# Kernel tuning notes

Measured on AMD Instinct MI355X. Metric: run time of the kernel, lower is better.

## Reference

```python
import jax, jax.numpy as jnp
import numpy as np

B, LQ, LK, D, H = 4, 1024, 1024, 512, 8


def setup_inputs() -> dict:
    key = jax.random.key(0)
    ks = jax.random.split(key, 6)
    # xavier_normal for (D, D): std = sqrt(2 / (D + D))
    std_qkv = (2.0 / (D + D)) ** 0.5
    std_p = (2.0 / (H * D + D)) ** 0.5
    x = jax.random.normal(ks[0], (B, LQ, D), dtype=jnp.float32)
    states = jax.random.normal(ks[1], (B, LK, D), dtype=jnp.float32)
    mask = jnp.ones((B, LQ, LK), dtype=jnp.int32)
    # per-head full-size QKV weights, stacked over heads: [H, D, D]
    Wq = jax.random.normal(ks[2], (H, D, D), dtype=jnp.float32) * std_qkv
    Wk = jax.random.normal(ks[3], (H, D, D), dtype=jnp.float32) * std_qkv
    Wv = jax.random.normal(ks[4], (H, D, D), dtype=jnp.float32) * std_qkv
    Wp = jax.random.normal(ks[5], (D, H * D), dtype=jnp.float32) * std_p
    return {"x": x, "states": states, "mask": mask,
            "Wq": Wq, "Wk": Wk, "Wv": Wv, "Wp": Wp}


def reference(x, states, mask, Wq, Wk, Wv, Wp):
    # Per-head linear projections (nn.Linear: y = x @ W.T), batched over heads.
    q = jnp.einsum('bld,hed->bhle', x, Wq)        # [B,H,Lq,D]
    k = jnp.einsum('bsd,hed->bhse', states, Wk)   # [B,H,Lk,D]
    v = jnp.einsum('bsd,hed->bhse', states, Wv)   # [B,H,Lk,D]
    scale = 1.0 / (D ** 0.5)
    scores = jnp.einsum('bhle,bhse->bhls', q, k) * scale  # [B,H,Lq,Lk]
    scores = jnp.where(mask[:, None, :, :] == 0, -jnp.inf, scores)
    attn = jax.nn.softmax(scores, axis=-1)
    # Original does broadcast multiply + sum; mathematically this is attn @ v.
    ctx = jnp.einsum('bhls,bhse->bhle', attn, v)  # [B,H,Lq,D]
    # torch.cat over heads in order -> head-major last dim
    ctx = jnp.transpose(ctx, (0, 2, 1, 3)).reshape(B, LQ, H * D)
    return ctx @ Wp.T  # [B,Lq,D]
```

## Files before the change

### kernel.cpp

```cpp
#include <hip/hip_runtime.h>
#include <hip/hip_bf16.h>
#include <cstdint>
#include <cstddef>


typedef __bf16 bf16;
typedef __bf16 bf16x4 __attribute__((ext_vector_type(4)));
typedef __bf16 bf16x8 __attribute__((ext_vector_type(8)));
typedef float f32x4 __attribute__((ext_vector_type(4)));

__device__ inline void gload_lds16(const void* g, void* l) {
  __builtin_amdgcn_global_load_lds(
      (const __attribute__((address_space(1))) void*)g,
      (__attribute__((address_space(3))) void*)l, 16, 0, 0);
}

template <typename CT, int MODE>
__device__ __forceinline__ void gemm_body(
    bf16* As, bf16* Bs,
    const bf16* __restrict__ A, const bf16* __restrict__ B, CT* __restrict__ C,
    int K, int lda, int ldb, int ldc, int m0, int n0, float scale,
    const unsigned* __restrict__ mrow, float* __restrict__ sumrow)
{
  const int t = threadIdx.x;
  const int lane = t & 63, w = t >> 6;
  const int wm = w >> 1, wn = w & 1;

  const int srow = t >> 3;
  const int schunk = (t & 7) ^ (srow & 7);
  const bf16* Ag = A + (size_t)(m0 + srow) * lda + schunk * 8;
  const bf16* Bg = B + (size_t)(n0 + srow) * ldb + schunk * 8;
  bf16* Als = As + t * 8;
  bf16* Bls = Bs + t * 8;

  f32x4 acc[4][4] = {};
  const int rr = lane & 15;
  const int q4 = lane >> 4;

  const int kIters = K >> 6;
  for (int kt = 0; kt < kIters; ++kt) {
    __syncthreads();
#pragma unroll
    for (int i = 0; i < 4; ++i) {
      gload_lds16(Ag + (size_t)(32 * i) * lda, Als + i * 2048);
      gload_lds16(Bg + (size_t)(32 * i) * ldb, Bls + i * 2048);
    }
    Ag += 64; Bg += 64;
    __syncthreads();

#pragma unroll
    for (int kk = 0; kk < 2; ++kk) {
      bf16x8 af[4], bfr[4];
      const int ck = kk * 4 + q4;
#pragma unroll
      for (int r = 0; r < 4; ++r) {
        const int R = wm * 64 + r * 16 + rr;
        af[r] = *(const bf16x8*)(As + R * 64 + ((ck ^ (R & 7)) << 3));
      }
#pragma unroll
      for (int c = 0; c < 4; ++c) {
        const int R = wn * 64 + c * 16 + rr;
        bfr[c] = *(const bf16x8*)(Bs + R * 64 + ((ck ^ (R & 7)) << 3));
      }
#pragma unroll
      for (int r = 0; r < 4; ++r)
#pragma unroll
        for (int c = 0; c < 4; ++c)
          acc[r][c] = __builtin_amdgcn_mfma_f32_16x16x32_bf16(af[r], bfr[c], acc[r][c], 0, 0, 0);
    }
  }

  if (MODE == 0) {
#pragma unroll
    for (int r = 0; r < 4; ++r) {
#pragma unroll
      for (int c = 0; c < 4; ++c) {
        const int gr0 = m0 + wm * 64 + r * 16 + (q4 << 2);
        const int gc = n0 + wn * 64 + c * 16 + rr;
#pragma unroll
        for (int i = 0; i < 4; ++i)
          C[(size_t)(gr0 + i) * ldc + gc] = (CT)(acc[r][c][i] * scale);
      }
    }
  } else {
    const int cb0 = (n0 + wn * 64) >> 5;
#pragma unroll
    for (int r = 0; r < 4; ++r) {
#pragma unroll
      for (int i = 0; i < 4; ++i) {
        const int row = m0 + wm * 64 + r * 16 + (q4 << 2) + i;
        const unsigned mw0 = mrow[(row << 5) + cb0];
        const unsigned mw1 = mrow[(row << 5) + cb0 + 1];
        float ps = 0.0f;
#pragma unroll
        for (int c = 0; c < 4; ++c) {
          const int gc = n0 + wn * 64 + c * 16 + rr;
          const unsigned mw = (c >= 2) ? mw1 : mw0;
          const unsigned bit = (mw >> (((c & 1) << 4) + rr)) & 1u;
          float p = bit ? __expf(acc[r][c][i] * scale) : 0.0f;
          C[(size_t)row * ldc + gc] = (CT)p;
          ps += p;
        }
        ps += __shfl_xor(ps, 1); ps += __shfl_xor(ps, 2);
        ps += __shfl_xor(ps, 4); ps += __shfl_xor(ps, 8);
        if (rr == 0) atomicAdd(sumrow + row, ps);
      }
    }
  }
}

__global__ __launch_bounds__(256) void prep_kernel(
    const float* __restrict__ x, const float* __restrict__ st,
    const float* __restrict__ Wp, const float* __restrict__ Wq,
    const float* __restrict__ Wk, const float* __restrict__ Wv,
    const int* __restrict__ mask,
    bf16* __restrict__ xb, bf16* __restrict__ stb, bf16* __restrict__ wpb,
    bf16* __restrict__ WqT, bf16* __restrict__ WkT, bf16* __restrict__ WvT,
    unsigned* __restrict__ mbits, float* __restrict__ sums)
{
  const int lin = blockIdx.x;
  const int t = threadIdx.x;
  if (lin < 6144) {
    const float* s; bf16* d;
    switch (lin >> 11) {
      case 0: s = x; d = xb; break;
      case 1: s = st; d = stb; break;
      default: s = Wp; d = wpb; break;
    }
    const int i = ((lin & 2047) * 256 + t) * 4;
    float4 v = *(const float4*)(s + i);
    bf16x4 o;
    o[0] = (bf16)v.x; o[1] = (bf16)v.y; o[2] = (bf16)v.z; o[3] = (bf16)v.w;
    *(bf16x4*)(d + i) = o;
  } else if (lin < 12288) {
    const int tid = lin - 6144;
    const float* s; bf16* d;
    switch (tid >> 11) {
      case 0: s = Wq; d = WqT; break;
      case 1: s = Wk; d = WkT; break;
      default: s = Wv; d = WvT; break;
    }
    const int gid = (tid & 2047) * 256 + t;
    const int e0 = (gid & 127) * 4;
    const int dd = (gid >> 7) & 511;
    const int h = gid >> 16;
    const float* src = s + (size_t)h * 262144 + (size_t)e0 * 512 + dd;
    bf16x4 o;
    o[0] = (bf16)src[0];
    o[1] = (bf16)src[512];
    o[2] = (bf16)src[1024];
    o[3] = (bf16)src[1536];
    *(bf16x4*)(d + (size_t)h * 262144 + (size_t)dd * 512 + e0) = o;
  } else if (lin < 12800) {
    const int gid = (lin - 12288) * 256 + t;
    const int* src = mask + (size_t)gid * 32;
    unsigned bits = 0;
#pragma unroll
    for (int j = 0; j < 32; j += 4) {
      int4 v = *(const int4*)(src + j);
      if (v.x) bits |= 1u << j;
      if (v.y) bits |= 1u << (j + 1);
      if (v.z) bits |= 1u << (j + 2);
      if (v.w) bits |= 1u << (j + 3);
    }
    mbits[gid] = bits;
  } else {
    const int i = ((lin - 12800) * 256 + t) * 4;
    *(float4*)(sums + i) = make_float4(0.f, 0.f, 0.f, 0.f);
  }
}

__global__ __launch_bounds__(256) void combine_kernel(
    const bf16* __restrict__ WqT, const bf16* __restrict__ WkT,
    const bf16* __restrict__ wpb, const bf16* __restrict__ WvT,
    bf16* __restrict__ Mt, bf16* __restrict__ U)
{
  __shared__ bf16 As[128 * 64];
  __shared__ bf16 Bs[128 * 64];
  const int bid = blockIdx.x;
  const int g = (bid & 7) * 32 + (bid >> 3);
  const int h = (g >> 4) & 7;
  const int tile = g & 15;
  if (g < 128) {
    gemm_body<bf16, 0>(As, Bs, WkT + (size_t)h * 262144, WqT + (size_t)h * 262144,
        Mt + (size_t)h * 262144, 512, 512, 512, 512,
        (tile >> 2) * 128, (tile & 3) * 128, 1.0f, nullptr, nullptr);
  } else {
    gemm_body<bf16, 0>(As, Bs, wpb + (size_t)h * 512, WvT + (size_t)h * 262144,
        U + (size_t)h * 262144, 512, 4096, 512, 512,
        (tile >> 2) * 128, (tile & 3) * 128, 1.0f, nullptr, nullptr);
  }
}

__global__ __launch_bounds__(256) void stage2_kernel(
    const bf16* __restrict__ xb, const bf16* __restrict__ stb,
    const bf16* __restrict__ Mt, const bf16* __restrict__ U,
    bf16* __restrict__ tq, bf16* __restrict__ VWT)
{
  __shared__ bf16 As[128 * 64];
  __shared__ bf16 Bs[128 * 64];
  const int bid = blockIdx.x;
  const int g = (bid & 7) * 256 + (bid >> 3);
  if (g < 1024) {
    const int z = g >> 5;
    const int tile = g & 31;
    const size_t zb = z >> 3, zh = z & 7;
    gemm_body<bf16, 0>(As, Bs, xb + zb * 524288, Mt + zh * 262144,
        tq + (size_t)z * 524288, 512, 512, 512, 512,
        (tile >> 2) * 128, (tile & 3) * 128, 1.0f, nullptr, nullptr);
  } else {
    const int g2 = g - 1024;
    const int z = g2 >> 5;
    const int j = g2 & 31;
    const size_t zb = z >> 3, zh = z & 7;
    gemm_body<bf16, 0>(As, Bs, U + zh * 262144, stb + zb * 524288,
        VWT + zb * 4194304 + zh * 524288, 512, 512, 512, 1024,
        (j >> 3) * 128, (j & 7) * 128, 1.0f, nullptr, nullptr);
  }
}

__global__ __launch_bounds__(256) void big_kernel(
    const bf16* __restrict__ tq, const bf16* __restrict__ stb,
    bf16* __restrict__ P,
    const unsigned* __restrict__ mbits, float* __restrict__ sums, float scale)
{
  __shared__ bf16 As[128 * 64];
  __shared__ bf16 Bs[128 * 64];
  const int bid = blockIdx.x;
  const int g = (bid & 7) * 256 + (bid >> 3);
  const int z = g >> 6;
  const int j = g & 63;
  const size_t zb = z >> 3, zh = z & 7;
  gemm_body<bf16, 1>(As, Bs,
      tq + (size_t)z * 524288,
      stb + zb * 524288,
      P + zb * 8388608 + zh * 1048576,
      512, 512, 512, 1024,
      (j >> 3) * 128, (j & 7) * 128, scale,
      mbits + (zb << 15), sums + ((size_t)z << 10));
}

__global__ __launch_bounds__(256) void pvw_kernel(
    const bf16* __restrict__ P, const bf16* __restrict__ VWT,
    const float* __restrict__ sums, float* __restrict__ part)
{
  __shared__ bf16 As[128 * 64];
  __shared__ bf16 Bs[128 * 64];
  const int lin = blockIdx.x;
  const int z = ((lin >> 8) << 3) | (lin & 7);
  const int j = (lin >> 3) & 31;
  const int zb = z >> 2, hp = z & 3;
  const int m0 = (j >> 2) * 128, n0 = (j & 3) * 128;
  const int t = threadIdx.x;
  const int lane = t & 63, w = t >> 6;
  const int wm = w >> 1, wn = w & 1;
  const int srow = t >> 3, schunk = (t & 7) ^ (srow & 7);
  const int rr = lane & 15, q4 = lane >> 4;
  bf16* Als = As + t * 8;
  bf16* Bls = Bs + t * 8;

  f32x4 accO[4][4] = {};

#pragma unroll
  for (int hh = 0; hh < 2; ++hh) {
    const int h = hp * 2 + hh;
    const bf16* Ag = P + (size_t)zb * 8388608 + (size_t)h * 1048576
                       + (size_t)(m0 + srow) * 1024 + schunk * 8;
    const bf16* Bg = VWT + (size_t)zb * 4194304 + (size_t)h * 524288
                        + (size_t)(n0 + srow) * 1024 + schunk * 8;
    f32x4 acc[4][4] = {};
    for (int kt = 0; kt < 16; ++kt) {
      __syncthreads();
#pragma unroll
      for (int i = 0; i < 4; ++i) {
        gload_lds16(Ag + (size_t)(32 * i) * 1024, Als + i * 2048);
        gload_lds16(Bg + (size_t)(32 * i) * 1024, Bls + i * 2048);
      }
      Ag += 64; Bg += 64;
      __syncthreads();
#pragma unroll
      for (int kk = 0; kk < 2; ++kk) {
        bf16x8 af[4], bfr[4];
        const int ck = kk * 4 + q4;
#pragma unroll
        for (int r = 0; r < 4; ++r) {
          const int R = wm * 64 + r * 16 + rr;
          af[r] = *(const bf16x8*)(As + R * 64 + ((ck ^ (R & 7)) << 3));
        }
#pragma unroll
        for (int c = 0; c < 4; ++c) {
          const int R = wn * 64 + c * 16 + rr;
          bfr[c] = *(const bf16x8*)(Bs + R * 64 + ((ck ^ (R & 7)) << 3));
        }
#pragma unroll
        for (int r = 0; r < 4; ++r)
#pragma unroll
          for (int c = 0; c < 4; ++c)
            acc[r][c] = __builtin_amdgcn_mfma_f32_16x16x32_bf16(af[r], bfr[c], acc[r][c], 0, 0, 0);
      }
    }
    const float* srs = sums + ((size_t)zb * 8 + h) * 1024;
#pragma unroll
    for (int r = 0; r < 4; ++r) {
#pragma unroll
      for (int i = 0; i < 4; ++i) {
        const float inv = 1.0f / srs[m0 + wm * 64 + r * 16 + (q4 << 2) + i];
#pragma unroll
        for (int c = 0; c < 4; ++c)
          accO[r][c][i] += acc[r][c][i] * inv;
      }
    }
  }

  float* Cp = part + (size_t)hp * 2097152 + (size_t)zb * 524288;
#pragma unroll
  for (int r = 0; r < 4; ++r) {
#pragma unroll
    for (int c = 0; c < 4; ++c) {
      const int gr0 = m0 + wm * 64 + r * 16 + (q4 << 2);
      const int gc = n0 + wn * 64 + c * 16 + rr;
#pragma unroll
      for (int i = 0; i < 4; ++i)
        Cp[(size_t)(gr0 + i) * 512 + gc] = accO[r][c][i];
    }
  }
}

__global__ __launch_bounds__(256) void reduce4(
    const float* __restrict__ part, float* __restrict__ out)
{
  const size_t i = ((size_t)blockIdx.x * 256 + threadIdx.x) * 4;
  float4 a = *(const float4*)(part + i);
  float4 b = *(const float4*)(part + 2097152 + i);
  float4 c = *(const float4*)(part + 4194304 + i);
  float4 d = *(const float4*)(part + 6291456 + i);
  float4 o;
  o.x = (a.x + b.x) + (c.x + d.x);
  o.y = (a.y + b.y) + (c.y + d.y);
  o.z = (a.z + b.z) + (c.z + d.z);
  o.w = (a.w + b.w) + (c.w + d.w);
  *(float4*)(out + i) = o;
}

extern "C" void kernel_launch(void* const* d_in, const int* in_sizes, int n_in,
                              void* d_out, int out_size, void* d_ws, size_t ws_size,
                              hipStream_t stream) {
  const float* x    = (const float*)d_in[0];
  const float* st   = (const float*)d_in[1];
  const int*   mask = (const int*)d_in[2];
  const float* Wq   = (const float*)d_in[3];
  const float* Wk   = (const float*)d_in[4];
  const float* Wv   = (const float*)d_in[5];
  const float* Wp   = (const float*)d_in[6];
  float* out = (float*)d_out;

  char* ws = (char*)d_ws;
  const size_t MB = 1048576;
  bf16* xb  = (bf16*)(ws);
  bf16* stb = (bf16*)(ws + 4 * MB);
  bf16* wpb = (bf16*)(ws + 8 * MB);
  bf16* WqT = (bf16*)(ws + 12 * MB);
  bf16* WkT = (bf16*)(ws + 16 * MB);
  bf16* WvT = (bf16*)(ws + 20 * MB);
  bf16* U   = (bf16*)(ws + 24 * MB);
  bf16* Mt  = (bf16*)(ws + 28 * MB);
  bf16* tq  = (bf16*)(ws + 32 * MB);
  bf16* VWT = (bf16*)(ws + 64 * MB);
  bf16* sc  = (bf16*)(ws + 96 * MB);
  unsigned* mbits = (unsigned*)(ws + 160 * MB);
  float*    sums  = (float*)(ws + 161 * MB);
  float*    part  = (float*)(ws + 32 * MB);

  dim3 blk(256);
  const float scale = 0.04419417382415922f;

  prep_kernel<<<dim3(12832), blk, 0, stream>>>(x, st, Wp, Wq, Wk, Wv, mask,
      xb, stb, wpb, WqT, WkT, WvT, mbits, sums);

  combine_kernel<<<dim3(256), blk, 0, stream>>>(WqT, WkT, wpb, WvT, Mt, U);

  stage2_kernel<<<dim3(2048), blk, 0, stream>>>(xb, stb, Mt, U, tq, VWT);

  big_kernel<<<dim3(2048), blk, 0, stream>>>(tq, stb, sc, mbits, sums, scale);

  pvw_kernel<<<dim3(512), blk, 0, stream>>>(sc, VWT, sums, part);

  reduce4<<<dim3(2048), blk, 0, stream>>>(part, out);
}
```

Before: 284.4 us.

## Fuse all six stages into one persistent cooperative kernel with grid syncs

Replaces the six separate kernel launches (prep, combine, stage2, big, pvw, reduce) with a single cooperative persistent kernel. Each stage's blocks become grid-stride loops and stages are separated by grid.sync(). The grid size comes from the occupancy query and is capped at 768 blocks. This removes launch gaps and inter-kernel drain/fill overhead. In exchange, the stages run with fewer resident blocks than before, which may lose the occupancy and tail behaviour of the separate launches. Grid-wide barriers also carry their own cost, and launch_bounds(256,3) may limit registers for the GEMM body.

```diff
diff --git a/kernel.cpp b/kernel.cpp
--- a/kernel.cpp
+++ b/kernel.cpp
@@ -1,4 +1,5 @@
 #include <hip/hip_runtime.h>
+#include <hip/hip_cooperative_groups.h>
 #include <hip/hip_bf16.h>
 #include <cstdint>
 #include <cstddef>
@@ -8,6 +9,8 @@
 typedef __bf16 bf16x4 __attribute__((ext_vector_type(4)));
 typedef __bf16 bf16x8 __attribute__((ext_vector_type(8)));
 typedef float f32x4 __attribute__((ext_vector_type(4)));
+
+namespace cg = cooperative_groups;
 
 __device__ inline void gload_lds16(const void* g, void* l) {
   __builtin_amdgcn_global_load_lds(
@@ -109,7 +112,8 @@
   }
 }
 
-__global__ __launch_bounds__(256) void prep_kernel(
+__device__ __forceinline__ void prep_work(
+    int lin,
     const float* __restrict__ x, const float* __restrict__ st,
     const float* __restrict__ Wp, const float* __restrict__ Wq,
     const float* __restrict__ Wk, const float* __restrict__ Wv,
@@ -118,7 +122,6 @@
     bf16* __restrict__ WqT, bf16* __restrict__ WkT, bf16* __restrict__ WvT,
     unsigned* __restrict__ mbits, float* __restrict__ sums)
 {
-  const int lin = blockIdx.x;
   const int t = threadIdx.x;
   if (lin < 6144) {
     const float* s; bf16* d;
@@ -133,14 +136,14 @@
     o[0] = (bf16)v.x; o[1] = (bf16)v.y; o[2] = (bf16)v.z; o[3] = (bf16)v.w;
     *(bf16x4*)(d + i) = o;
   } else if (lin < 12288) {
-    const int tid = lin - 6144;
+    const int tid2 = lin - 6144;
     const float* s; bf16* d;
-    switch (tid >> 11) {
+    switch (tid2 >> 11) {
       case 0: s = Wq; d = WqT; break;
       case 1: s = Wk; d = WkT; break;
       default: s = Wv; d = WvT; break;
     }
-    const int gid = (tid & 2047) * 256 + t;
+    const int gid = (tid2 & 2047) * 256 + t;
     const int e0 = (gid & 127) * 4;
     const int dd = (gid >> 7) & 511;
     const int h = gid >> 16;
@@ -170,83 +173,11 @@
   }
 }
 
-__global__ __launch_bounds__(256) void combine_kernel(
-    const bf16* __restrict__ WqT, const bf16* __restrict__ WkT,
-    const bf16* __restrict__ wpb, const bf16* __restrict__ WvT,
-    bf16* __restrict__ Mt, bf16* __restrict__ U)
-{
-  __shared__ bf16 As[128 * 64];
-  __shared__ bf16 Bs[128 * 64];
-  const int bid = blockIdx.x;
-  const int g = (bid & 7) * 32 + (bid >> 3);
-  const int h = (g >> 4) & 7;
-  const int tile = g & 15;
-  if (g < 128) {
-    gemm_body<bf16, 0>(As, Bs, WkT + (size_t)h * 262144, WqT + (size_t)h * 262144,
-        Mt + (size_t)h * 262144, 512, 512, 512, 512,
-        (tile >> 2) * 128, (tile & 3) * 128, 1.0f, nullptr, nullptr);
-  } else {
-    gemm_body<bf16, 0>(As, Bs, wpb + (size_t)h * 512, WvT + (size_t)h * 262144,
-        U + (size_t)h * 262144, 512, 4096, 512, 512,
-        (tile >> 2) * 128, (tile & 3) * 128, 1.0f, nullptr, nullptr);
-  }
-}
-
-__global__ __launch_bounds__(256) void stage2_kernel(
-    const bf16* __restrict__ xb, const bf16* __restrict__ stb,
-    const bf16* __restrict__ Mt, const bf16* __restrict__ U,
-    bf16* __restrict__ tq, bf16* __restrict__ VWT)
-{
-  __shared__ bf16 As[128 * 64];
-  __shared__ bf16 Bs[128 * 64];
-  const int bid = blockIdx.x;
-  const int g = (bid & 7) * 256 + (bid >> 3);
-  if (g < 1024) {
-    const int z = g >> 5;
-    const int tile = g & 31;
-    const size_t zb = z >> 3, zh = z & 7;
-    gemm_body<bf16, 0>(As, Bs, xb + zb * 524288, Mt + zh * 262144,
-        tq + (size_t)z * 524288, 512, 512, 512, 512,
-        (tile >> 2) * 128, (tile & 3) * 128, 1.0f, nullptr, nullptr);
-  } else {
-    const int g2 = g - 1024;
-    const int z = g2 >> 5;
-    const int j = g2 & 31;
-    const size_t zb = z >> 3, zh = z & 7;
-    gemm_body<bf16, 0>(As, Bs, U + zh * 262144, stb + zb * 524288,
-        VWT + zb * 4194304 + zh * 524288, 512, 512, 512, 1024,
-        (j >> 3) * 128, (j & 7) * 128, 1.0f, nullptr, nullptr);
-  }
-}
-
-__global__ __launch_bounds__(256) void big_kernel(
-    const bf16* __restrict__ tq, const bf16* __restrict__ stb,
-    bf16* __restrict__ P,
-    const unsigned* __restrict__ mbits, float* __restrict__ sums, float scale)
-{
-  __shared__ bf16 As[128 * 64];
-  __shared__ bf16 Bs[128 * 64];
-  const int bid = blockIdx.x;
-  const int g = (bid & 7) * 256 + (bid >> 3);
-  const int z = g >> 6;
-  const int j = g & 63;
-  const size_t zb = z >> 3, zh = z & 7;
-  gemm_body<bf16, 1>(As, Bs,
-      tq + (size_t)z * 524288,
-      stb + zb * 524288,
-      P + zb * 8388608 + zh * 1048576,
-      512, 512, 512, 1024,
-      (j >> 3) * 128, (j & 7) * 128, scale,
-      mbits + (zb << 15), sums + ((size_t)z << 10));
-}
-
-__global__ __launch_bounds__(256) void pvw_kernel(
+__device__ __forceinline__ void pvw_work(
+    int lin, bf16* As, bf16* Bs,
     const bf16* __restrict__ P, const bf16* __restrict__ VWT,
     const float* __restrict__ sums, float* __restrict__ part)
 {
-  __shared__ bf16 As[128 * 64];
-  __shared__ bf16 Bs[128 * 64];
-  const int lin = blockIdx.x;
   const int z = ((lin >> 8) << 3) | (lin & 7);
   const int j = (lin >> 3) & 31;
   const int zb = z >> 2, hp = z & 3;
@@ -326,20 +257,98 @@
   }
 }
 
-__global__ __launch_bounds__(256) void reduce4(
-    const float* __restrict__ part, float* __restrict__ out)
+__global__ __launch_bounds__(256, 3) void fused_kernel(
+    const float* __restrict__ x, const float* __restrict__ st,
+    const int* __restrict__ mask,
+    const float* __restrict__ Wq, const float* __restrict__ Wk,
+    const float* __restrict__ Wv, const float* __restrict__ Wp,
+    bf16* __restrict__ xb, bf16* __restrict__ stb, bf16* __restrict__ wpb,
+    bf16* __restrict__ WqT, bf16* __restrict__ WkT, bf16* __restrict__ WvT,
+    bf16* __restrict__ U, bf16* __restrict__ Mt,
+    bf16* __restrict__ tq, bf16* __restrict__ VWT, bf16* __restrict__ P,
+    unsigned* __restrict__ mbits, float* __restrict__ sums,
+    float* __restrict__ part, float* __restrict__ out, float scale)
 {
-  const size_t i = ((size_t)blockIdx.x * 256 + threadIdx.x) * 4;
-  float4 a = *(const float4*)(part + i);
-  float4 b = *(const float4*)(part + 2097152 + i);
-  float4 c = *(const float4*)(part + 4194304 + i);
-  float4 d = *(const float4*)(part + 6291456 + i);
-  float4 o;
-  o.x = (a.x + b.x) + (c.x + d.x);
-  o.y = (a.y + b.y) + (c.y + d.y);
-  o.z = (a.z + b.z) + (c.z + d.z);
-  o.w = (a.w + b.w) + (c.w + d.w);
-  *(float4*)(out + i) = o;
+  __shared__ bf16 As[128 * 64];
+  __shared__ bf16 Bs[128 * 64];
+  cg::grid_group grid = cg::this_grid();
+  const int bid = blockIdx.x;
+  const int G = gridDim.x;
+
+  for (int j = bid; j < 12832; j += G)
+    prep_work(j, x, st, Wp, Wq, Wk, Wv, mask,
+              xb, stb, wpb, WqT, WkT, WvT, mbits, sums);
+  grid.sync();
+
+  for (int j = bid; j < 256; j += G) {
+    const int g = (j & 7) * 32 + (j >> 3);
+    const int h = (g >> 4) & 7;
+    const int tile = g & 15;
+    if (g < 128) {
+      gemm_body<bf16, 0>(As, Bs, WkT + (size_t)h * 262144, WqT + (size_t)h * 262144,
+          Mt + (size_t)h * 262144, 512, 512, 512, 512,
+          (tile >> 2) * 128, (tile & 3) * 128, 1.0f, nullptr, nullptr);
+    } else {
+      gemm_body<bf16, 0>(As, Bs, wpb + (size_t)h * 512, WvT + (size_t)h * 262144,
+          U + (size_t)h * 262144, 512, 4096, 512, 512,
+          (tile >> 2) * 128, (tile & 3) * 128, 1.0f, nullptr, nullptr);
+    }
+  }
+  grid.sync();
+
+  for (int j = bid; j < 2048; j += G) {
+    const int g = (j & 7) * 256 + (j >> 3);
+    if (g < 1024) {
+      const int z = g >> 5;
+      const int tile = g & 31;
+      const size_t zb = z >> 3, zh = z & 7;
+      gemm_body<bf16, 0>(As, Bs, xb + zb * 524288, Mt + zh * 262144,
+          tq + (size_t)z * 524288, 512, 512, 512, 512,
+          (tile >> 2) * 128, (tile & 3) * 128, 1.0f, nullptr, nullptr);
+    } else {
+      const int g2 = g - 1024;
+      const int z = g2 >> 5;
+      const int jj = g2 & 31;
+      const size_t zb = z >> 3, zh = z & 7;
+      gemm_body<bf16, 0>(As, Bs, U + zh * 262144, stb + zb * 524288,
+          VWT + zb * 4194304 + zh * 524288, 512, 512, 512, 1024,
+          (jj >> 3) * 128, (jj & 7) * 128, 1.0f, nullptr, nullptr);
+    }
+  }
+  grid.sync();
+
+  for (int j = bid; j < 2048; j += G) {
+    const int g = (j & 7) * 256 + (j >> 3);
+    const int z = g >> 6;
+    const int jj = g & 63;
+    const size_t zb = z >> 3, zh = z & 7;
+    gemm_body<bf16, 1>(As, Bs,
+        tq + (size_t)z * 524288,
+        stb + zb * 524288,
+        P + zb * 8388608 + zh * 1048576,
+        512, 512, 512, 1024,
+        (jj >> 3) * 128, (jj & 7) * 128, scale,
+        mbits + (zb << 15), sums + ((size_t)z << 10));
+  }
+  grid.sync();
+
+  for (int j = bid; j < 512; j += G)
+    pvw_work(j, As, Bs, P, VWT, sums, part);
+  grid.sync();
+
+  for (int i4 = bid * 256 + (int)threadIdx.x; i4 < 524288; i4 += G * 256) {
+    const size_t i = (size_t)i4 * 4;
+    float4 a = *(const float4*)(part + i);
+    float4 b = *(const float4*)(part + 2097152 + i);
+    float4 c = *(const float4*)(part + 4194304 + i);
+    float4 d = *(const float4*)(part + 6291456 + i);
+    float4 o;
+    o.x = (a.x + b.x) + (c.x + d.x);
+    o.y = (a.y + b.y) + (c.y + d.y);
+    o.z = (a.z + b.z) + (c.z + d.z);
+    o.w = (a.w + b.w) + (c.w + d.w);
+    *(float4*)(out + i) = o;
+  }
 }
 
 extern "C" void kernel_launch(void* const* d_in, const int* in_sizes, int n_in,
@@ -366,24 +375,29 @@
   bf16* Mt  = (bf16*)(ws + 28 * MB);
   bf16* tq  = (bf16*)(ws + 32 * MB);
   bf16* VWT = (bf16*)(ws + 64 * MB);
-  bf16* sc  = (bf16*)(ws + 96 * MB);
+  bf16* P   = (bf16*)(ws + 96 * MB);
   unsigned* mbits = (unsigned*)(ws + 160 * MB);
   float*    sums  = (float*)(ws + 161 * MB);
   float*    part  = (float*)(ws + 32 * MB);
 
-  dim3 blk(256);
-  const float scale = 0.04419417382415922f;
-
-  prep_kernel<<<dim3(12832), blk, 0, stream>>>(x, st, Wp, Wq, Wk, Wv, mask,
-      xb, stb, wpb, WqT, WkT, WvT, mbits, sums);
-
-  combine_kernel<<<dim3(256), blk, 0, stream>>>(WqT, WkT, wpb, WvT, Mt, U);
-
-  stage2_kernel<<<dim3(2048), blk, 0, stream>>>(xb, stb, Mt, U, tq, VWT);
-
-  big_kernel<<<dim3(2048), blk, 0, stream>>>(tq, stb, sc, mbits, sums, scale);
-
-  pvw_kernel<<<dim3(512), blk, 0, stream>>>(sc, VWT, sums, part);
-
-  reduce4<<<dim3(2048), blk, 0, stream>>>(part, out);
-}
+  float scale = 0.04419417382415922f;
+
+  int nb = 0;
+  hipError_t e = hipOccupancyMaxActiveBlocksPerMultiprocessor(
+      &nb, (const void*)fused_kernel, 256, 0);
+  if (e != hipSuccess || nb < 1) nb = 1;
+  int grid = nb * 256;
+  if (grid > 768) grid = 768;
+  grid &= ~7;
+  if (grid < 8) grid = 8;
+
+  void* args[] = {
+    (void*)&x, (void*)&st, (void*)&mask, (void*)&Wq, (void*)&Wk,
+    (void*)&Wv, (void*)&Wp,
+    (void*)&xb, (void*)&stb, (void*)&wpb, (void*)&WqT, (void*)&WkT,
+    (void*)&WvT, (void*)&U, (void*)&Mt, (void*)&tq, (void*)&VWT, (void*)&P,
+    (void*)&mbits, (void*)&sums, (void*)&part, (void*)&out, (void*)&scale
+  };
+  hipLaunchCooperativeKernel((const void*)fused_kernel, dim3(grid), dim3(256),
+                             args, 0, stream);
+}
```

New measurement: 627.3 us. 2.21x slower.
